# Kernel optimization log

Hardware: AMD Instinct MI355X
Metric: run time of the kernel (lower is better)

Reference implementation:

```python
import jax, jax.numpy as jnp
import numpy as np

B, S, XDIM, YDIM = 64, 1024, 256, 128


def setup_inputs() -> dict:
    key = jax.random.key(0)
    ks = jax.random.split(key, 7)
    q = jax.random.normal(ks[0], (B, S, XDIM), dtype=jnp.float32)
    # Linear weights in torch layout [out, in]; biases [out]
    sc = 1.0 / np.sqrt(XDIM)
    Wq = jax.random.normal(ks[1], (YDIM, XDIM), dtype=jnp.float32) * sc
    Wk = jax.random.normal(ks[2], (YDIM, XDIM), dtype=jnp.float32) * sc
    Wv = jax.random.normal(ks[3], (YDIM, XDIM), dtype=jnp.float32) * sc
    bq = jax.random.normal(ks[4], (YDIM,), dtype=jnp.float32) * sc
    bk = jax.random.normal(ks[5], (YDIM,), dtype=jnp.float32) * sc
    bv = jax.random.normal(ks[6], (YDIM,), dtype=jnp.float32) * sc
    return {"q": q, "Wq": Wq, "bq": bq, "Wk": Wk, "bk": bk, "Wv": Wv, "bv": bv}


def reference(q, Wq, bq, Wk, bk, Wv, bv):
    # Q, K, V projections: [B, S, YDIM]
    Q = jnp.einsum('bsx,yx->bsy', q, Wq) + bq
    K = jnp.einsum('bsx,yx->bsy', q, Wk) + bk
    V = jnp.einsum('bsx,yx->bsy', q, Wv) + bv
    scale = jnp.float32(np.sqrt(YDIM))
    # scores [B, S_q, S_k]; softmax over the QUERY axis (dim=-2), non-standard
    scores = jnp.einsum('bqd,bkd->bqk', Q, K) / scale
    attn = jax.nn.softmax(scores, axis=-2)
    out = jnp.einsum('bqk,bkd->bqd', attn, V)  # [B, S, YDIM]
    # flat=True: max over dim=-2 -> [B, YDIM]
    return jnp.max(out, axis=-2)
```

## Files before the change

### kernel.cpp

```cpp
#include <hip/hip_runtime.h>

typedef __bf16 bf16;
typedef __attribute__((ext_vector_type(8))) __bf16 bf16x8;
typedef __attribute__((ext_vector_type(4))) __bf16 bf16x4;
typedef __attribute__((ext_vector_type(4))) float  f32x4;

static __device__ __forceinline__ f32x4 mfma16(bf16x8 a, bf16x8 b, f32x4 c) {
  return __builtin_amdgcn_mfma_f32_16x16x32_bf16(a, b, c, 0, 0, 0);
}
static __device__ __forceinline__ float fexp2(float x) {
  return __builtin_amdgcn_exp2f(x);
}
static __device__ __forceinline__ float flog2(float x) {
  return __builtin_amdgcn_logf(x);
}

#define EXP_C1 (1.4426950408889634f / 11.313708498984760f)

typedef const __attribute__((address_space(1))) unsigned int gas_u32;
typedef __attribute__((address_space(3))) unsigned int las_u32;
#define GLDS16(gp, lp) __builtin_amdgcn_global_load_lds((gas_u32*)(gp), (las_u32*)(lp), 16, 0, 0)

#define WAITN0() __asm__ volatile("s_waitcnt vmcnt(0)" ::: "memory")


__global__ __launch_bounds__(256) void k_prep(
    const float* __restrict__ Wq, const float* __restrict__ Wk,
    const float* __restrict__ Wv, bf16* __restrict__ Wc, float* __restrict__ out)
{
  int id = blockIdx.x * 256 + threadIdx.x;
  if (id < 8192) out[id] = -__builtin_inff();
  int proj = id >> 12, r = id & 4095;
  int g = r >> 7, n = r & 127;
  const float* W = proj == 0 ? Wq : proj == 1 ? Wk : Wv;
  const float sc = (proj == 0) ? EXP_C1 : 1.0f;
  const float4* src = (const float4*)(W + n * 256 + g * 8);
  float4 a = src[0], b = src[1];
  bf16x8 o = { (bf16)(a.x * sc), (bf16)(a.y * sc), (bf16)(a.z * sc), (bf16)(a.w * sc),
               (bf16)(b.x * sc), (bf16)(b.y * sc), (bf16)(b.z * sc), (bf16)(b.w * sc) };
  *(bf16x8*)(Wc + (size_t)proj * 32768 + g * 1024 + n * 8) = o;
}

__global__ __launch_bounds__(512, 2) void k_qkv(
    const float* __restrict__ q, const bf16* __restrict__ Wc,
    const float* __restrict__ bq, const float* __restrict__ bk, const float* __restrict__ bv,
    bf16* __restrict__ Qb, bf16* __restrict__ Kb, bf16* __restrict__ VT)
{
  __shared__ char Alf[2][65536];

  const int tid = threadIdx.x, lane = tid & 63, wave = tid >> 6;
  const int ln = lane & 15, quad = lane >> 4;
  const int wr = wave >> 2, wc = wave & 3;
  const int tile0 = blockIdx.x * 4;

#define STAGE(bi, tile) do {                                                     \
    const char* src_ = (const char*)(q + (size_t)(tile) * 16384);                \
    char* d_ = Alf[bi];                                                          \
    for (int c = 0; c < 8; ++c) {                                                \
      int ch = wave * 8 + c;                                                     \
      GLDS16(src_ + ch * 1024 + ((lane * 16) ^ ((ch & 7) << 4)),                 \
             d_ + ch * 1024);                                                    \
    }                                                                            \
  } while (0)

  STAGE(0, tile0);

  for (int it = 0; it < 4; ++it) {
    WAITN0();
    __syncthreads();
    if (it < 3) STAGE((it + 1) & 1, tile0 + it + 1);
    const char* Bf = Alf[it & 1];

    const int m0 = (tile0 + it) * 64;
    const int b = m0 >> 10, st = (m0 & 1023) >> 7, s_off = m0 & 64;
    const size_t tbase = ((size_t)b * 8 + st) * 16384;

    f32x4 aQ[2][2] = {}, aK[2][2] = {}, aV[2][2] = {};
    for (int kk = 0; kk < 8; ++kk) {
      int g = kk * 4 + quad;
      bf16x8 ax[2];
      for (int t = 0; t < 2; ++t) {
        int r = wr * 32 + t * 16 + ln;
        int cb = g * 32, sw = (r & 7) << 4;
        f32x4 a0 = *(const f32x4*)(Bf + r * 1024 + (cb ^ sw));
        f32x4 a1 = *(const f32x4*)(Bf + r * 1024 + ((cb + 16) ^ sw));
        ax[t] = bf16x8{ (bf16)a0[0], (bf16)a0[1], (bf16)a0[2], (bf16)a0[3],
                        (bf16)a1[0], (bf16)a1[1], (bf16)a1[2], (bf16)a1[3] };
      }
      bf16x8 bwQ[2], bwK[2], bwV[2];
      for (int t2 = 0; t2 < 2; ++t2) {
        const int off = g * 1024 + (wc * 32 + t2 * 16 + ln) * 8;
        bwQ[t2] = *(const bf16x8*)(Wc + off);
        bwK[t2] = *(const bf16x8*)(Wc + 32768 + off);
        bwV[t2] = *(const bf16x8*)(Wc + 65536 + off);
      }
      __builtin_amdgcn_s_setprio(1);
      for (int i = 0; i < 2; ++i)
        for (int j = 0; j < 2; ++j) {
          aQ[i][j] = mfma16(bwQ[i], ax[j], aQ[i][j]);
          aK[i][j] = mfma16(bwK[i], ax[j], aK[i][j]);
        }
      for (int i = 0; i < 2; ++i)
        for (int j = 0; j < 2; ++j)
          aV[i][j] = mfma16(ax[i], bwV[j], aV[i][j]);
      __builtin_amdgcn_s_setprio(0);
    }

    for (int p = 0; p < 2; ++p) {
      bf16* dst = (p == 0 ? Qb : Kb) + tbase;
      const float* bias = p == 0 ? bq : bk;
      for (int i = 0; i < 2; ++i) {
        float4 b4 = *(const float4*)&bias[wc * 32 + i * 16 + quad * 4];
        if (p == 0) { b4.x *= EXP_C1; b4.y *= EXP_C1; b4.z *= EXP_C1; b4.w *= EXP_C1; }
        int gd = wc * 4 + i * 2 + (quad >> 1);
        int e0 = (quad & 1) * 4;
        for (int j = 0; j < 2; ++j) {
          int s = s_off + wr * 32 + j * 16 + ln;
          const f32x4 a_ = p == 0 ? aQ[i][j] : aK[i][j];
          bf16x4 o = { (bf16)(a_[0] + b4.x), (bf16)(a_[1] + b4.y),
                       (bf16)(a_[2] + b4.z), (bf16)(a_[3] + b4.w) };
          *(bf16x4*)&dst[(size_t)gd * 1024 + (size_t)s * 8 + e0] = o;
        }
      }
    }
    {
      bf16* dst = VT + tbase;
      for (int j = 0; j < 2; ++j) {
        int d = wc * 32 + j * 16 + ln;
        float bb = bv[d];
        for (int i = 0; i < 2; ++i) {
          int s0 = s_off + wr * 32 + i * 16 + quad * 4;
          int G  = (s0 >> 5) * 4 + ((s0 & 15) >> 2);
          int e0 = (s0 & 16) >> 2;
          bf16x4 o = { (bf16)(aV[i][j][0] + bb), (bf16)(aV[i][j][1] + bb),
                       (bf16)(aV[i][j][2] + bb), (bf16)(aV[i][j][3] + bb) };
          *(bf16x4*)&dst[(size_t)G * 1024 + (size_t)d * 8 + e0] = o;
        }
      }
    }
  }
#undef STAGE
}

__global__ __launch_bounds__(256, 2) void k_stats(
    const bf16* __restrict__ Qb, const bf16* __restrict__ Kb, float* __restrict__ nlg)
{
  __shared__ char Qbuf[2][32768];
  const int b = blockIdx.x, kt = blockIdx.y;
  const int tid = threadIdx.x, lane = tid & 63, wave = tid >> 6;
  const int ln = lane & 15, quad = lane >> 4;

  const bf16* ktile = Kb + ((size_t)b * 8 + kt) * 16384;
  bf16x8 ak[2][4];
  for (int i = 0; i < 2; ++i)
    for (int kk = 0; kk < 4; ++kk)
      ak[i][kk] = *(const bf16x8*)(ktile + (kk * 4 + quad) * 1024 + (wave * 32 + i * 16 + ln) * 8);

  const char* qb_b = (const char*)(Qb + (size_t)b * 8 * 16384);
  for (int c = 0; c < 8; ++c)
    GLDS16(qb_b + (wave * 8 + c) * 1024 + lane * 16, &Qbuf[0][(wave * 8 + c) * 1024]);

  f32x4 csum[2] = {};
  for (int qt = 0; qt < 8; ++qt) {
    WAITN0();
    __syncthreads();
    if (qt < 7)
      for (int c = 0; c < 8; ++c)
        GLDS16(qb_b + (size_t)(qt + 1) * 32768 + (wave * 8 + c) * 1024 + lane * 16,
               &Qbuf[(qt + 1) & 1][(wave * 8 + c) * 1024]);
    const char* Ql = Qbuf[qt & 1];
    for (int jq = 0; jq < 8; ++jq) {
      f32x4 s0 = {}, s1 = {};
      __builtin_amdgcn_s_setprio(1);
      for (int kk = 0; kk < 4; ++kk) {
        bf16x8 bqf = *(const bf16x8*)(Ql + ((kk * 4 + quad) * 2 + (jq >> 2)) * 1024
                                         + ((jq * 16 + ln) & 63) * 16);
        s0 = mfma16(ak[0][kk], bqf, s0);
        s1 = mfma16(ak[1][kk], bqf, s1);
      }
      __builtin_amdgcn_s_setprio(0);
      for (int rr = 0; rr < 4; ++rr) {
        csum[0][rr] += fexp2(s0[rr]);
        csum[1][rr] += fexp2(s1[rr]);
      }
    }
  }
  for (int i = 0; i < 2; ++i)
    for (int rr = 0; rr < 4; ++rr) {
      float v = csum[i][rr];
      v += __shfl_xor(v, 1, 64); v += __shfl_xor(v, 2, 64);
      v += __shfl_xor(v, 4, 64); v += __shfl_xor(v, 8, 64);
      csum[i][rr] = v;
    }
  if (ln == 0) {
    float* dst = nlg + (size_t)b * 1024 + kt * 128 + wave * 32 + quad * 4;
    for (int i = 0; i < 2; ++i)
      for (int rr = 0; rr < 4; ++rr)
        dst[i * 16 + rr] = -flog2(csum[i][rr]);
  }
}

__global__ __launch_bounds__(256, 2) void k_attn(
    const bf16* __restrict__ Qb, const bf16* __restrict__ Kb, const bf16* __restrict__ VT,
    const float* __restrict__ nlg, float* __restrict__ out)
{
  __shared__ char bufK[2][16384];
  __shared__ char bufV[2][16384];
  __shared__ float nll[1024];
  __shared__ float redm[4][128];

  const int b = blockIdx.x, qt = blockIdx.y;
  const int tid = threadIdx.x, lane = tid & 63, wave = tid >> 6;
  const int ln = lane & 15, quad = lane >> 4;

  *(float4*)&nll[tid * 4] = *(const float4*)(nlg + (size_t)b * 1024 + tid * 4);

  const bf16* qtile = Qb + ((size_t)b * 8 + qt) * 16384;
  bf16x8 bq_[2][4];
  for (int j = 0; j < 2; ++j)
    for (int kk = 0; kk < 4; ++kk)
      bq_[j][kk] = *(const bf16x8*)(qtile + (kk * 4 + quad) * 1024 + (wave * 32 + j * 16 + ln) * 8);

  const char* kb_b = (const char*)(Kb + (size_t)b * 8 * 16384);
  const char* vt_b = (const char*)(VT + (size_t)b * 8 * 16384);

#define K_DMA(t) do {                                                            \
    const char* ksrc = kb_b + (size_t)((t) >> 1) * 32768 + ((t) & 1) * 1024;     \
    char* dk = bufK[(t) & 1];                                                    \
    for (int c = 0; c < 4; ++c) {                                                \
      int ch = wave * 4 + c;                                                     \
      GLDS16(ksrc + ch * 2048 + lane * 16, dk + ch * 1024);                      \
    }                                                                            \
  } while (0)
#define V_DMA(t) do {                                                            \
    const char* vsrc = vt_b + (size_t)((t) >> 1) * 32768 + ((t) & 1) * 16384;    \
    char* dv = bufV[(t) & 1];                                                    \
    for (int c = 0; c < 4; ++c) {                                                \
      int ch = wave * 4 + c;                                                     \
      GLDS16(vsrc + (ch >> 1) * 2048 + (ch & 1) * 1024 + lane * 16,              \
             dv + ch * 1024);                                                    \
    }                                                                            \
  } while (0)

#define QK(tt, SN) do {                                                          \
    const char* Kl = bufK[(tt) & 1];                                             \
    _Pragma("unroll")                                                            \
    for (int i = 0; i < 4; ++i) {                                                \
      float4 L4 = *(float4*)&nll[(tt) * 64 + i * 16 + quad * 4];                 \
      f32x4 ini = { L4.x, L4.y, L4.z, L4.w };                                    \
      SN[i][0] = ini; SN[i][1] = ini;                                            \
    }                                                                            \
    __builtin_amdgcn_s_setprio(1);                                               \
    _Pragma("unroll")                                                            \
    for (int kk = 0; kk < 4; ++kk) {                                             \
      bf16x8 ak[4];                                                              \
      _Pragma("unroll")                                                          \
      for (int i = 0; i < 4; ++i)                                                \
        ak[i] = *(const bf16x8*)(Kl + (kk * 4 + quad) * 1024 + (i * 16 + ln) * 16); \
      _Pragma("unroll")                                                          \
      for (int i = 0; i < 4; ++i) {                                              \
        SN[i][0] = mfma16(ak[i], bq_[0][kk], SN[i][0]);                          \
        SN[i][1] = mfma16(ak[i], bq_[1][kk], SN[i][1]);                          \
      }                                                                          \
    }                                                                            \
    __builtin_amdgcn_s_setprio(0);                                               \
  } while (0)

#define EXPPV(tt, SC) do {                                                       \
    const char* Vl = bufV[(tt) & 1];                                             \
    _Pragma("unroll")                                                            \
    for (int s = 0; s < 2; ++s) {                                                \
      f32x4 lo0 = SC[2 * s][0], hi0 = SC[2 * s + 1][0];                          \
      f32x4 lo1 = SC[2 * s][1], hi1 = SC[2 * s + 1][1];                          \
      bf16x8 pf0 = bf16x8{                                                       \
        (bf16)fexp2(lo0[0]), (bf16)fexp2(lo0[1]), (bf16)fexp2(lo0[2]), (bf16)fexp2(lo0[3]), \
        (bf16)fexp2(hi0[0]), (bf16)fexp2(hi0[1]), (bf16)fexp2(hi0[2]), (bf16)fexp2(hi0[3]) }; \
      bf16x8 pf1 = bf16x8{                                                       \
        (bf16)fexp2(lo1[0]), (bf16)fexp2(lo1[1]), (bf16)fexp2(lo1[2]), (bf16)fexp2(lo1[3]), \
        (bf16)fexp2(hi1[0]), (bf16)fexp2(hi1[1]), (bf16)fexp2(hi1[2]), (bf16)fexp2(hi1[3]) }; \
      _Pragma("unroll")                                                          \
      for (int j2 = 0; j2 < 8; ++j2) {                                           \
        bf16x8 bv_ = *(const bf16x8*)(Vl + ((s * 4 + quad) * 2 + (j2 >> 2)) * 1024 \
                                         + ((j2 * 16 + ln) & 63) * 16);          \
        oacc[0][j2] = mfma16(pf0, bv_, oacc[0][j2]);                             \
        oacc[1][j2] = mfma16(pf1, bv_, oacc[1][j2]);                             \
      }                                                                          \
    }                                                                            \
  } while (0)

#define STEP(t, CUR, NXT) do {                                                   \
    WAITN0();                                                                    \
    __syncthreads();                                                             \
    if ((t) < 14) K_DMA((t) + 2);                                                \
    if ((t) < 15) V_DMA((t) + 1);                                                \
    if ((t) < 15) QK((t) + 1, NXT);                                              \
    EXPPV((t), CUR);                                                             \
  } while (0)

  f32x4 oacc[2][8] = {};
  f32x4 sA[4][2], sB[4][2];

  K_DMA(0);
  WAITN0();
  __syncthreads();
  K_DMA(1); V_DMA(0);
  QK(0, sA);

  for (int tp = 0; tp < 8; ++tp) {
    STEP(2 * tp,     sA, sB);
    STEP(2 * tp + 1, sB, sA);
  }
#undef STEP
#undef EXPPV
#undef QK
#undef K_DMA
#undef V_DMA

  for (int j2 = 0; j2 < 8; ++j2) {
    float m = -3.4e38f;
    for (int j = 0; j < 2; ++j)
      for (int rr = 0; rr < 4; ++rr)
        m = fmaxf(m, oacc[j][j2][rr]);
    m = fmaxf(m, __shfl_xor(m, 16, 64));
    m = fmaxf(m, __shfl_xor(m, 32, 64));
    if (lane < 16) redm[wave][j2 * 16 + ln] = m;
  }
  __syncthreads();
  if (tid < 128) {
    float m = fmaxf(fmaxf(redm[0][tid], redm[1][tid]), fmaxf(redm[2][tid], redm[3][tid]));
    float* addr = out + (size_t)b * 128 + tid;
    if (m >= 0.0f) atomicMax((int*)addr, __float_as_int(m));
    else           atomicMin((unsigned int*)addr, __float_as_uint(m));
  }
}

extern "C" void kernel_launch(void* const* d_in, const int* in_sizes, int n_in,
                              void* d_out, int out_size, void* d_ws, size_t ws_size,
                              hipStream_t stream) {
  const float* q  = (const float*)d_in[0];
  const float* Wq = (const float*)d_in[1];
  const float* bq = (const float*)d_in[2];
  const float* Wk = (const float*)d_in[3];
  const float* bk = (const float*)d_in[4];
  const float* Wv = (const float*)d_in[5];
  const float* bv = (const float*)d_in[6];
  float* out = (float*)d_out;

  char* ws = (char*)d_ws;
  bf16*  Qb    = (bf16*)(ws);
  bf16*  Kb    = (bf16*)(ws + (16u << 20));
  bf16*  VT    = (bf16*)(ws + (32u << 20));
  float* nlg   = (float*)(ws + (48u << 20));
  bf16*  Wc    = (bf16*)(ws + (49u << 20));

  k_prep <<<48,           256, 0, stream>>>(Wq, Wk, Wv, Wc, out);
  k_qkv  <<<dim3(256),    512, 0, stream>>>(q, Wc, bq, bk, bv, Qb, Kb, VT);
  k_stats<<<dim3(64, 8),  256, 0, stream>>>(Qb, Kb, nlg);
  k_attn <<<dim3(64, 8),  256, 0, stream>>>(Qb, Kb, VT, nlg, out);
}
```

Before: 93.68 us.

## Drop LDS staging in QKV projection; load q directly from global with smaller blocks

The QKV projection kernel stops staging q tiles through double-buffered LDS with async global-to-LDS loads. It now reads fp32 q rows straight from global memory into registers, one 64-row tile per 256-thread block, with 1024 blocks in place of 256 persistent blocks of 512 threads. Each wave now covers all 64 rows for its 32 output columns, so the four waves of a block each read the same q data from global/L2 rather than sharing it through LDS. The aim is more occupancy and no LDS or barrier overhead, at the cost of redundant global reads and less coalesced row-strided loads.

Measured after the change: 107.5 us. +14.7%, slower.

```diff
diff --git a/kernel.cpp b/kernel.cpp
--- a/kernel.cpp
+++ b/kernel.cpp
@@ -41,105 +41,88 @@
   *(bf16x8*)(Wc + (size_t)proj * 32768 + g * 1024 + n * 8) = o;
 }
 
-__global__ __launch_bounds__(512, 2) void k_qkv(
+__global__ __launch_bounds__(256, 3) void k_qkv(
     const float* __restrict__ q, const bf16* __restrict__ Wc,
     const float* __restrict__ bq, const float* __restrict__ bk, const float* __restrict__ bv,
     bf16* __restrict__ Qb, bf16* __restrict__ Kb, bf16* __restrict__ VT)
 {
-  __shared__ char Alf[2][65536];
-
   const int tid = threadIdx.x, lane = tid & 63, wave = tid >> 6;
   const int ln = lane & 15, quad = lane >> 4;
-  const int wr = wave >> 2, wc = wave & 3;
-  const int tile0 = blockIdx.x * 4;
-
-#define STAGE(bi, tile) do {                                                     \
-    const char* src_ = (const char*)(q + (size_t)(tile) * 16384);                \
-    char* d_ = Alf[bi];                                                          \
-    for (int c = 0; c < 8; ++c) {                                                \
-      int ch = wave * 8 + c;                                                     \
-      GLDS16(src_ + ch * 1024 + ((lane * 16) ^ ((ch & 7) << 4)),                 \
-             d_ + ch * 1024);                                                    \
-    }                                                                            \
-  } while (0)
-
-  STAGE(0, tile0);
-
-  for (int it = 0; it < 4; ++it) {
-    WAITN0();
-    __syncthreads();
-    if (it < 3) STAGE((it + 1) & 1, tile0 + it + 1);
-    const char* Bf = Alf[it & 1];
-
-    const int m0 = (tile0 + it) * 64;
-    const int b = m0 >> 10, st = (m0 & 1023) >> 7, s_off = m0 & 64;
-    const size_t tbase = ((size_t)b * 8 + st) * 16384;
-
-    f32x4 aQ[2][2] = {}, aK[2][2] = {}, aV[2][2] = {};
-    for (int kk = 0; kk < 8; ++kk) {
-      int g = kk * 4 + quad;
-      bf16x8 ax[2];
-      for (int t = 0; t < 2; ++t) {
-        int r = wr * 32 + t * 16 + ln;
-        int cb = g * 32, sw = (r & 7) << 4;
-        f32x4 a0 = *(const f32x4*)(Bf + r * 1024 + (cb ^ sw));
-        f32x4 a1 = *(const f32x4*)(Bf + r * 1024 + ((cb + 16) ^ sw));
-        ax[t] = bf16x8{ (bf16)a0[0], (bf16)a0[1], (bf16)a0[2], (bf16)a0[3],
-                        (bf16)a1[0], (bf16)a1[1], (bf16)a1[2], (bf16)a1[3] };
-      }
-      bf16x8 bwQ[2], bwK[2], bwV[2];
-      for (int t2 = 0; t2 < 2; ++t2) {
-        const int off = g * 1024 + (wc * 32 + t2 * 16 + ln) * 8;
-        bwQ[t2] = *(const bf16x8*)(Wc + off);
-        bwK[t2] = *(const bf16x8*)(Wc + 32768 + off);
-        bwV[t2] = *(const bf16x8*)(Wc + 65536 + off);
-      }
-      __builtin_amdgcn_s_setprio(1);
-      for (int i = 0; i < 2; ++i)
-        for (int j = 0; j < 2; ++j) {
-          aQ[i][j] = mfma16(bwQ[i], ax[j], aQ[i][j]);
-          aK[i][j] = mfma16(bwK[i], ax[j], aK[i][j]);
-        }
-      for (int i = 0; i < 2; ++i)
-        for (int j = 0; j < 2; ++j)
-          aV[i][j] = mfma16(ax[i], bwV[j], aV[i][j]);
-      __builtin_amdgcn_s_setprio(0);
-    }
-
-    for (int p = 0; p < 2; ++p) {
-      bf16* dst = (p == 0 ? Qb : Kb) + tbase;
-      const float* bias = p == 0 ? bq : bk;
-      for (int i = 0; i < 2; ++i) {
-        float4 b4 = *(const float4*)&bias[wc * 32 + i * 16 + quad * 4];
-        if (p == 0) { b4.x *= EXP_C1; b4.y *= EXP_C1; b4.z *= EXP_C1; b4.w *= EXP_C1; }
-        int gd = wc * 4 + i * 2 + (quad >> 1);
-        int e0 = (quad & 1) * 4;
-        for (int j = 0; j < 2; ++j) {
-          int s = s_off + wr * 32 + j * 16 + ln;
-          const f32x4 a_ = p == 0 ? aQ[i][j] : aK[i][j];
-          bf16x4 o = { (bf16)(a_[0] + b4.x), (bf16)(a_[1] + b4.y),
-                       (bf16)(a_[2] + b4.z), (bf16)(a_[3] + b4.w) };
-          *(bf16x4*)&dst[(size_t)gd * 1024 + (size_t)s * 8 + e0] = o;
-        }
-      }
-    }
-    {
-      bf16* dst = VT + tbase;
-      for (int j = 0; j < 2; ++j) {
-        int d = wc * 32 + j * 16 + ln;
-        float bb = bv[d];
-        for (int i = 0; i < 2; ++i) {
-          int s0 = s_off + wr * 32 + i * 16 + quad * 4;
-          int G  = (s0 >> 5) * 4 + ((s0 & 15) >> 2);
-          int e0 = (s0 & 16) >> 2;
-          bf16x4 o = { (bf16)(aV[i][j][0] + bb), (bf16)(aV[i][j][1] + bb),
-                       (bf16)(aV[i][j][2] + bb), (bf16)(aV[i][j][3] + bb) };
-          *(bf16x4*)&dst[(size_t)G * 1024 + (size_t)d * 8 + e0] = o;
-        }
-      }
-    }
-  }
-#undef STAGE
+  const int wc = wave;
+  const int m0 = blockIdx.x * 64;
+  const float* qt = q + (size_t)m0 * 256;
+
+  const int b = m0 >> 10, st = (m0 & 1023) >> 7, s_off = m0 & 64;
+  const size_t tbase = ((size_t)b * 8 + st) * 16384;
+
+  f32x4 aQ[2][4] = {}, aK[2][4] = {}, aV[4][2] = {};
+  #pragma unroll
+  for (int kk = 0; kk < 8; ++kk) {
+    bf16x8 ax[4];
+    #pragma unroll
+    for (int t = 0; t < 4; ++t) {
+      const float* rp = qt + (size_t)(t * 16 + ln) * 256 + kk * 32 + quad * 8;
+      float4 a0 = *(const float4*)rp;
+      float4 a1 = *(const float4*)(rp + 4);
+      ax[t] = bf16x8{ (bf16)a0.x, (bf16)a0.y, (bf16)a0.z, (bf16)a0.w,
+                      (bf16)a1.x, (bf16)a1.y, (bf16)a1.z, (bf16)a1.w };
+    }
+    bf16x8 bwQ[2], bwK[2], bwV[2];
+    #pragma unroll
+    for (int t2 = 0; t2 < 2; ++t2) {
+      const int off = (kk * 4 + quad) * 1024 + (wc * 32 + t2 * 16 + ln) * 8;
+      bwQ[t2] = *(const bf16x8*)(Wc + off);
+      bwK[t2] = *(const bf16x8*)(Wc + 32768 + off);
+      bwV[t2] = *(const bf16x8*)(Wc + 65536 + off);
+    }
+    __builtin_amdgcn_s_setprio(1);
+    #pragma unroll
+    for (int i = 0; i < 2; ++i)
+      #pragma unroll
+      for (int j = 0; j < 4; ++j) {
+        aQ[i][j] = mfma16(bwQ[i], ax[j], aQ[i][j]);
+        aK[i][j] = mfma16(bwK[i], ax[j], aK[i][j]);
+      }
+    #pragma unroll
+    for (int i = 0; i < 4; ++i)
+      #pragma unroll
+      for (int j = 0; j < 2; ++j)
+        aV[i][j] = mfma16(ax[i], bwV[j], aV[i][j]);
+    __builtin_amdgcn_s_setprio(0);
+  }
+
+  for (int p = 0; p < 2; ++p) {
+    bf16* dst = (p == 0 ? Qb : Kb) + tbase;
+    const float* bias = p == 0 ? bq : bk;
+    for (int i = 0; i < 2; ++i) {
+      float4 b4 = *(const float4*)&bias[wc * 32 + i * 16 + quad * 4];
+      if (p == 0) { b4.x *= EXP_C1; b4.y *= EXP_C1; b4.z *= EXP_C1; b4.w *= EXP_C1; }
+      int gd = wc * 4 + i * 2 + (quad >> 1);
+      int e0 = (quad & 1) * 4;
+      for (int j = 0; j < 4; ++j) {
+        int s = s_off + j * 16 + ln;
+        const f32x4 a_ = p == 0 ? aQ[i][j] : aK[i][j];
+        bf16x4 o = { (bf16)(a_[0] + b4.x), (bf16)(a_[1] + b4.y),
+                     (bf16)(a_[2] + b4.z), (bf16)(a_[3] + b4.w) };
+        *(bf16x4*)&dst[(size_t)gd * 1024 + (size_t)s * 8 + e0] = o;
+      }
+    }
+  }
+  {
+    bf16* dst = VT + tbase;
+    for (int j = 0; j < 2; ++j) {
+      int d = wc * 32 + j * 16 + ln;
+      float bb = bv[d];
+      for (int i = 0; i < 4; ++i) {
+        int s0 = s_off + i * 16 + quad * 4;
+        int G  = (s0 >> 5) * 4 + ((s0 & 15) >> 2);
+        int e0 = (s0 & 16) >> 2;
+        bf16x4 o = { (bf16)(aV[i][j][0] + bb), (bf16)(aV[i][j][1] + bb),
+                     (bf16)(aV[i][j][2] + bb), (bf16)(aV[i][j][3] + bb) };
+        *(bf16x4*)&dst[(size_t)G * 1024 + (size_t)d * 8 + e0] = o;
+      }
+    }
+  }
 }
 
 __global__ __launch_bounds__(256, 2) void k_stats(
@@ -354,7 +337,7 @@
   bf16*  Wc    = (bf16*)(ws + (49u << 20));
 
   k_prep <<<48,           256, 0, stream>>>(Wq, Wk, Wv, Wc, out);
-  k_qkv  <<<dim3(256),    512, 0, stream>>>(q, Wc, bq, bk, bv, Qb, Kb, VT);
+  k_qkv  <<<dim3(1024),   256, 0, stream>>>(q, Wc, bq, bk, bv, Qb, Kb, VT);
   k_stats<<<dim3(64, 8),  256, 0, stream>>>(Qb, Kb, nlg);
   k_attn <<<dim3(64, 8),  256, 0, stream>>>(Qb, Kb, VT, nlg, out);
 }
```
